# Optimization experiments

Measured on AMD Instinct MI355X. Metric: run time of the kernel, lower is better.

Reference implementation:

```python
import jax, jax.numpy as jnp
import numpy as np

D_MODEL, D_STATE, D_CONV, D_INNER = 1024, 16, 4, 2048
BATCH, SEQ = 4, 2048


def silu(v):
    return v * jax.nn.sigmoid(v)


def setup_inputs() -> dict:
    key = jax.random.key(0)
    ks = jax.random.split(key, 7)
    x = jax.random.normal(ks[0], (BATCH, SEQ, D_MODEL), dtype=jnp.float32)
    s = 0.02
    W_in = jax.random.normal(ks[1], (D_MODEL, 2 * D_INNER), dtype=jnp.float32) * s
    conv_w = jax.random.normal(ks[2], (D_INNER, 1, D_CONV), dtype=jnp.float32) * s  # depthwise (O, I/g=1, K)
    conv_b = jax.random.normal(ks[3], (D_INNER,), dtype=jnp.float32) * s
    W_xproj = jax.random.normal(ks[4], (D_INNER, 2 * D_STATE + 1), dtype=jnp.float32) * s
    A_log = jnp.log(jnp.tile(jnp.arange(1, D_STATE + 1, dtype=jnp.float32), (D_INNER, 1)))
    D = jnp.ones((D_INNER,), dtype=jnp.float32)
    W_out = jax.random.normal(ks[5], (D_INNER, D_MODEL), dtype=jnp.float32) * s
    return {"x": x, "W_in": W_in, "conv_w": conv_w, "conv_b": conv_b,
            "W_xproj": W_xproj, "A_log": A_log, "D": D, "W_out": W_out}


def reference(x, W_in, conv_w, conv_b, W_xproj, A_log, D, W_out):
    B, L, _ = x.shape
    xz = x @ W_in                                   # (B, L, 2*d_inner)
    x_proj, z = jnp.split(xz, 2, axis=-1)
    # Depthwise causal conv: padding=d_conv-1 then truncate to L == left-pad only.
    xc = jax.lax.conv_general_dilated(
        x_proj.transpose(0, 2, 1), conv_w,
        window_strides=(1,), padding=[(D_CONV - 1, 0)],
        feature_group_count=D_INNER,
        dimension_numbers=("NCH", "OIH", "NCH"))
    x_conv = silu((xc + conv_b[None, :, None]).transpose(0, 2, 1))  # (B, L, d_inner)
    ssm = x_conv @ W_xproj                           # (B, L, 1+2*d_state)
    delta = jax.nn.softplus(ssm[..., 0])             # (B, L)
    Bm = ssm[..., 1:1 + D_STATE]                     # (B, L, d_state)
    Cm = ssm[..., 1 + D_STATE:]                      # (B, L, d_state)
    # Original: deltaA = exp(delta*A) and softmax weights are computed but unused.
    deltaB = delta[..., None] * Bm                   # (B, L, d_state)
    # h_approx = mean_L(x outer deltaB): avoid (B,L,d_inner,d_state) intermediate.
    h_mean = jnp.einsum("bld,bln->bdn", x_conv, deltaB) / L  # (B, d_inner, d_state)
    y = jnp.einsum("bdn,bln->bld", h_mean, Cm)       # (B, L, d_inner)
    y = y + D[None, None, :] * x_conv
    y = y * silu(z)
    return y @ W_out                                 # (B, L, d_model)
```

## Files before the change

kernel.cpp:

```cpp
#include <hip/hip_runtime.h>
#include <hip/hip_bf16.h>
#include <stdint.h>

typedef __bf16 bf16x8 __attribute__((ext_vector_type(8)));
typedef float f32x4 __attribute__((ext_vector_type(4)));
typedef unsigned short u16;
typedef u16 ushort4v __attribute__((ext_vector_type(4)));
typedef u16 ushort8v __attribute__((ext_vector_type(8)));

__device__ __forceinline__ u16 f2bf(float f) {
    union { float f; uint32_t u; } v; v.f = f;
    uint32_t u = v.u + 0x7FFFu + ((v.u >> 16) & 1u);
    return (u16)(u >> 16);
}
__device__ __forceinline__ float bf2f(u16 b) {
    union { uint32_t u; float f; } v; v.u = ((uint32_t)b) << 16;
    return v.f;
}
__device__ __forceinline__ float silu_f(float v) {
    return v / (1.0f + __expf(-v));
}
__device__ __forceinline__ void gload_lds16(const u16* g, u16* l) {
    __builtin_amdgcn_global_load_lds(
        (const __attribute__((address_space(1))) void*)g,
        (__attribute__((address_space(3))) void*)l, 16, 0, 0);
}

__global__ void cvt_bf16_k(const float* __restrict__ src, u16* __restrict__ dst, int n4) {
    int i = blockIdx.x * 256 + threadIdx.x;
    if (i < n4) {
        float4 v = *(const float4*)&src[(int64_t)i * 4];
        ushort4v o = { f2bf(v.x), f2bf(v.y), f2bf(v.z), f2bf(v.w) };
        *(ushort4v*)&dst[(int64_t)i * 4] = o;
    }
}

__global__ __launch_bounds__(256) void trans_cvt_k(
        const float* __restrict__ src, u16* __restrict__ dst, int R, int C) {
    __shared__ float t[32][33];
    const int bc = blockIdx.x, br = blockIdx.y;
    const int tx = threadIdx.x & 31, ty = threadIdx.x >> 5;
#pragma unroll
    for (int i = 0; i < 4; i++) {
        int r = ty + i * 8;
        t[r][tx] = src[(int64_t)(br * 32 + r) * C + bc * 32 + tx];
    }
    __syncthreads();
#pragma unroll
    for (int i = 0; i < 4; i++) {
        int c = ty + i * 8;
        dst[(int64_t)(bc * 32 + c) * R + br * 32 + tx] = f2bf(t[tx][c]);
    }
}

__global__ void prep_wxt_k(const float* __restrict__ wx, u16* __restrict__ wxt) {
    int idx = blockIdx.x * 256 + threadIdx.x;
    if (idx < 48 * 2048) {
        int j = idx >> 11, d = idx & 2047;
        wxt[idx] = (j < 33) ? f2bf(wx[d * 33 + j]) : (u16)0;
    }
}

template<int M_REP, int WARPS_M, int B_HALVES, bool OUT_BF16>
__global__ __launch_bounds__(512) void gemm_dp(
        const u16* __restrict__ A, const u16* __restrict__ Bt,
        void* __restrict__ Cout, int nbn_sh, int NT, int lda, int ldb, int ldc) {
    constexpr int WARPS_N = 8 / WARPS_M;
    constexpr int QPT = M_REP / 2;
    constexpr int WV_M = M_REP * 16;
    constexpr int BN = WARPS_N * 64;
    constexpr int B_T = BN * 64;

    __shared__ __align__(16) u16 As[2 * 16384];
    __shared__ __align__(16) u16 Bs[2 * B_T];

    const int tid = threadIdx.x;
    const int wave = tid >> 6;
    const int lane = tid & 63;
    const int wm = wave / WARPS_N, wn = wave % WARPS_N;
    const int fr = lane & 15, fq = lane >> 4;

    const int nwg = gridDim.x;
    const int cpx = nwg >> 3;
    const int swz = (blockIdx.x & 7) * cpx + (blockIdx.x >> 3);
    const int bm = swz >> nbn_sh;
    const int bn = swz & ((1 << nbn_sh) - 1);

    const int srow = tid >> 3;
    const int scol8 = ((tid & 7) ^ (srow & 7)) * 8;
    const u16* gA = A + (int64_t)(bm * 256 + srow) * lda + scol8;
    const u16* gB = Bt + (int64_t)(bn * BN + srow) * ldb + scol8;
    const int64_t lda64 = lda, ldb64 = ldb;

    const int ksw0 = ((fq) ^ (fr & 7)) * 8;
    const int ksw1 = ((4 + fq) ^ (fr & 7)) * 8;
    const int arow0 = (wm * WV_M + fr) * 64;
    const int brow0 = (wn * 64 + fr) * 64;

    auto STAGE_A = [&](int kt, int buf) {
#pragma unroll
        for (int h = 0; h < 2; ++h)
#pragma unroll
            for (int j = 0; j < 2; ++j)
                gload_lds16(gA + (int64_t)(h * 128 + j * 64) * lda64 + kt * 64,
                            &As[buf * 16384 + h * 8192 + j * 4096 + tid * 8]);
    };
    auto STAGE_B_HALF = [&](int kt, int buf, int h) {
#pragma unroll
        for (int j = 0; j < 2; ++j)
            gload_lds16(gB + (int64_t)(h * 128 + j * 64) * ldb64 + kt * 64,
                        &Bs[buf * B_T + h * 8192 + j * 4096 + tid * 8]);
    };

    f32x4 acc[M_REP][4] = {};

    STAGE_A(0, 0);
#pragma unroll
    for (int h = 0; h < B_HALVES; ++h) STAGE_B_HALF(0, 0, h);
#pragma unroll
    for (int h = 0; h < B_HALVES; ++h) STAGE_B_HALF(1, 1, h);
    if constexpr (B_HALVES == 2) { asm volatile("s_waitcnt vmcnt(4)" ::: "memory"); }
    else                         { asm volatile("s_waitcnt vmcnt(2)" ::: "memory"); }
    __builtin_amdgcn_s_barrier();

    const int NI = NT >> 1;
    for (int s = 0; s < NI; ++s) {
        const bool more = (s + 1 < NI);
        const int kt2 = 2 * s + 2, kt3 = 2 * s + 3;
#pragma unroll
        for (int t = 0; t < 2; ++t) {
            const u16* Ab = &As[t * 16384];
            const u16* Bb = &Bs[t * B_T];
            bf16x8 breg[4][2];
#pragma unroll
            for (int q = 0; q < QPT; ++q) {
                if (q == 0) {
#pragma unroll
                    for (int n = 0; n < 4; ++n) {
                        breg[n][0] = *(const bf16x8*)(Bb + brow0 + n * 1024 + ksw0);
                        breg[n][1] = *(const bf16x8*)(Bb + brow0 + n * 1024 + ksw1);
                    }
                }
                bf16x8 areg[2][2];
#pragma unroll
                for (int j = 0; j < 2; ++j) {
                    areg[j][0] = *(const bf16x8*)(Ab + arow0 + (2 * q + j) * 1024 + ksw0);
                    areg[j][1] = *(const bf16x8*)(Ab + arow0 + (2 * q + j) * 1024 + ksw1);
                }
                if constexpr (QPT == 4) {
                    if (t == 0 && q == 0)         STAGE_A(2 * s + 1, 1);
                    if (t == 0 && q == 2 && more) STAGE_B_HALF(kt2, 0, 0);
                    if (t == 0 && q == 3 && more) STAGE_B_HALF(kt2, 0, 1);
                    if (t == 1 && q == 0 && more) STAGE_A(kt2, 0);
                    if (t == 1 && q == 2 && more) STAGE_B_HALF(kt3, 1, 0);
                    if (t == 1 && q == 3 && more) STAGE_B_HALF(kt3, 1, 1);
                } else {
                    if (t == 0 && q == 0)         STAGE_A(2 * s + 1, 1);
                    if (t == 0 && q == 1 && more) STAGE_B_HALF(kt2, 0, 0);
                    if (t == 1 && q == 0 && more) STAGE_A(kt2, 0);
                    if (t == 1 && q == 1 && more) STAGE_B_HALF(kt3, 1, 0);
                }
                __builtin_amdgcn_s_barrier();
                asm volatile("s_waitcnt lgkmcnt(0)" ::: "memory");
                __builtin_amdgcn_sched_barrier(0);
                __builtin_amdgcn_s_setprio(1);
#pragma unroll
                for (int j = 0; j < 2; ++j)
#pragma unroll
                    for (int n = 0; n < 4; ++n) {
                        acc[2 * q + j][n] = __builtin_amdgcn_mfma_f32_16x16x32_bf16(
                            areg[j][0], breg[n][0], acc[2 * q + j][n], 0, 0, 0);
                        acc[2 * q + j][n] = __builtin_amdgcn_mfma_f32_16x16x32_bf16(
                            areg[j][1], breg[n][1], acc[2 * q + j][n], 0, 0, 0);
                    }
                __builtin_amdgcn_s_setprio(0);
                __builtin_amdgcn_sched_barrier(0);
                if (q == QPT - 1) {
                    if (more) {
                        if constexpr (B_HALVES == 2) { asm volatile("s_waitcnt vmcnt(4)" ::: "memory"); }
                        else                         { asm volatile("s_waitcnt vmcnt(2)" ::: "memory"); }
                    } else {
                        asm volatile("s_waitcnt vmcnt(0)" ::: "memory");
                    }
                }
                __builtin_amdgcn_s_barrier();
            }
        }
    }

#pragma unroll
    for (int m = 0; m < M_REP; ++m) {
#pragma unroll
        for (int n = 0; n < 4; ++n) {
            const int col = bn * BN + wn * 64 + n * 16 + fr;
#pragma unroll
            for (int r = 0; r < 4; ++r) {
                const int row = bm * 256 + wm * WV_M + m * 16 + fq * 4 + r;
                if constexpr (OUT_BF16)
                    ((u16*)Cout)[(int64_t)row * ldc + col] = f2bf(acc[m][n][r]);
                else
                    ((float*)Cout)[(int64_t)row * ldc + col] = acc[m][n][r];
            }
        }
    }
}

__global__ __launch_bounds__(256) void conv_silu_k(
        const u16* __restrict__ xz, const float* __restrict__ cw,
        const float* __restrict__ cb, u16* __restrict__ xc) {
    const int blk = blockIdx.x;
    const int b = blk >> 9;
    const int l0 = (blk & 511) << 2;
    const int d0 = threadIdx.x * 8;
    float w[8][4], bias[8];
#pragma unroll
    for (int j = 0; j < 8; j++) {
        float4 wv = *(const float4*)&cw[(d0 + j) * 4];
        w[j][0] = wv.x; w[j][1] = wv.y; w[j][2] = wv.z; w[j][3] = wv.w;
        bias[j] = cb[d0 + j];
    }
    float xp[7][8];
#pragma unroll
    for (int r = 0; r < 7; r++) {
        int l = l0 - 3 + r;
        if (l < 0) {
#pragma unroll
            for (int j = 0; j < 8; j++) xp[r][j] = 0.f;
        } else {
            ushort8v v = *(const ushort8v*)&xz[((int64_t)(b * 2048 + l)) * 4096 + d0];
#pragma unroll
            for (int j = 0; j < 8; j++) xp[r][j] = bf2f(v[j]);
        }
    }
#pragma unroll
    for (int li = 0; li < 4; li++) {
        ushort8v o;
#pragma unroll
        for (int j = 0; j < 8; j++) {
            float s = bias[j];
#pragma unroll
            for (int k = 0; k < 4; k++) s += w[j][k] * xp[li + k][j];
            o[j] = f2bf(silu_f(s));
        }
        *(ushort8v*)&xc[((int64_t)(b * 2048 + l0 + li)) * 2048 + d0] = o;
    }
}

__global__ __launch_bounds__(256) void ssm_proj_k(
        const u16* __restrict__ xc, const u16* __restrict__ wxt,
        float* __restrict__ spart) {
    const int gw = (blockIdx.x << 2) + (threadIdx.x >> 6);
    const int lane = threadIdx.x & 63;
    const int rb = gw >> 2, kc = gw & 3;
    const int fr = lane & 15, fq = lane >> 4;
    const u16* ap = xc + (int64_t)(rb * 16 + fr) * 2048 + kc * 512 + fq * 8;
    const u16* bp = wxt + (int64_t)fr * 2048 + kc * 512 + fq * 8;
    f32x4 acc0 = {}, acc1 = {}, acc2 = {};
#pragma unroll 4
    for (int k = 0; k < 512; k += 32) {
        bf16x8 av = *(const bf16x8*)(ap + k);
        bf16x8 b0 = *(const bf16x8*)(bp + k);
        bf16x8 b1 = *(const bf16x8*)(bp + 16 * 2048 + k);
        bf16x8 b2 = *(const bf16x8*)(bp + 32 * 2048 + k);
        acc0 = __builtin_amdgcn_mfma_f32_16x16x32_bf16(av, b0, acc0, 0, 0, 0);
        acc1 = __builtin_amdgcn_mfma_f32_16x16x32_bf16(av, b1, acc1, 0, 0, 0);
        acc2 = __builtin_amdgcn_mfma_f32_16x16x32_bf16(av, b2, acc2, 0, 0, 0);
    }
    float* sp = spart + ((int64_t)kc * 8192 + rb * 16) * 48;
#pragma unroll
    for (int r = 0; r < 4; r++) {
        int ro = (fq * 4 + r) * 48;
        sp[ro + fr] = acc0[r];
        sp[ro + 16 + fr] = acc1[r];
        sp[ro + 32 + fr] = acc2[r];
    }
}

__global__ __launch_bounds__(256) void ssm_fin_k(
        const float* __restrict__ spart, float* __restrict__ dB,
        float* __restrict__ Cm) {
    const int row = blockIdx.x * 256 + threadIdx.x;
    const float* sp = spart + (int64_t)row * 48;
    float s[33];
#pragma unroll
    for (int j = 0; j < 33; j++)
        s[j] = sp[j] + sp[8192 * 48 + j] + sp[2 * 8192 * 48 + j] + sp[3 * 8192 * 48 + j];
    float d0v = s[0];
    float delta = (d0v > 20.f) ? d0v : log1pf(__expf(d0v));
#pragma unroll
    for (int n = 0; n < 16; n++) {
        dB[(int64_t)row * 16 + n] = delta * s[1 + n] * (1.0f / 2048.0f);
        Cm[(int64_t)row * 16 + n] = s[17 + n];
    }
}

__global__ __launch_bounds__(256) void h_part_k(
        const u16* __restrict__ xc, const float* __restrict__ dB,
        float* __restrict__ hp) {
    const int blk = blockIdx.x;
    const int dt = blk & 7, b = (blk >> 3) & 3, lc = blk >> 5;
    const int d = dt * 256 + threadIdx.x;
    const u16* xp = xc + ((int64_t)(b * 2048 + lc * 256)) * 2048 + d;
    const float* dbp = dB + (int64_t)(b * 2048 + lc * 256) * 16;
    float acc[16] = {};
    for (int l = 0; l < 256; l++) {
        float xv = bf2f(xp[(int64_t)l * 2048]);
#pragma unroll
        for (int n = 0; n < 16; n++) acc[n] += xv * dbp[l * 16 + n];
    }
    float* o = hp + ((int64_t)((lc * 4 + b) * 2048 + d)) * 16;
#pragma unroll
    for (int n = 0; n < 16; n++) o[n] = acc[n];
}

__global__ void h_red_k(const float* __restrict__ hp, float* __restrict__ h) {
    const int i = blockIdx.x * 256 + threadIdx.x;
    float s = 0.f;
#pragma unroll
    for (int c = 0; c < 8; c++) s += hp[(int64_t)c * 131072 + i];
    h[i] = s;
}

__global__ __launch_bounds__(256) void y_gate_k(
        u16* __restrict__ xz, const u16* __restrict__ xc,
        const float* __restrict__ h, const float* __restrict__ Cm,
        const float* __restrict__ Dp) {
    const int blk = blockIdx.x;
    const int lc = blk & 63, dt = (blk >> 6) & 1, b = blk >> 7;
    const int d0 = dt * 1024 + threadIdx.x * 4;
    const float* hpp = h + ((int64_t)(b * 2048 + d0)) * 16;
    float hreg[4][16];
#pragma unroll
    for (int i = 0; i < 4; i++)
#pragma unroll
        for (int n = 0; n < 16; n++) hreg[i][n] = hpp[i * 16 + n];
    float Dv[4];
#pragma unroll
    for (int i = 0; i < 4; i++) Dv[i] = Dp[d0 + i];
    __shared__ float Cs[32][16];
    if (threadIdx.x < 128)
        ((float4*)&Cs[0][0])[threadIdx.x] =
            ((const float4*)(Cm + (int64_t)(b * 2048 + lc * 32) * 16))[threadIdx.x];
    __syncthreads();
    for (int li = 0; li < 32; li++) {
        const int64_t rowz = (int64_t)(b * 2048 + lc * 32 + li);
        ushort4v xcv = *(const ushort4v*)&xc[rowz * 2048 + d0];
        ushort4v zv = *(const ushort4v*)&xz[rowz * 4096 + 2048 + d0];
        ushort4v o;
#pragma unroll
        for (int i = 0; i < 4; i++) {
            float s = Dv[i] * bf2f(xcv[i]);
#pragma unroll
            for (int n = 0; n < 16; n++) s += hreg[i][n] * Cs[li][n];
            o[i] = f2bf(s * silu_f(bf2f(zv[i])));
        }
        *(ushort4v*)&xz[rowz * 4096 + d0] = o;
    }
}

extern "C" void kernel_launch(void* const* d_in, const int* in_sizes, int n_in,
                              void* d_out, int out_size, void* d_ws, size_t ws_size,
                              hipStream_t stream) {
    (void)in_sizes; (void)n_in; (void)out_size; (void)ws_size;
    const float* x      = (const float*)d_in[0];
    const float* W_in   = (const float*)d_in[1];
    const float* conv_w = (const float*)d_in[2];
    const float* conv_b = (const float*)d_in[3];
    const float* W_xp   = (const float*)d_in[4];
    const float* Dp     = (const float*)d_in[6];
    const float* W_out  = (const float*)d_in[7];
    float* out = (float*)d_out;
    char* ws = (char*)d_ws;

    u16*   x_bf   = (u16*)(ws);
    float* spart  = (float*)(ws);
    float* dB     = (float*)(ws + 6291456);
    float* Cm     = (float*)(ws + 6815744);
    float* hp     = (float*)(ws + 7340032);
    float* h      = (float*)(ws + 11534336);
    u16*   Wt_in  = (u16*)(ws + 16777216);
    u16*   Wt_out = (u16*)(ws + 25165824);
    u16*   Wxt    = (u16*)(ws + 29360128);
    u16*   xz     = (u16*)(ws + 29556736);
    u16*   xcv    = (u16*)(ws + 96665600);

    cvt_bf16_k<<<8192, 256, 0, stream>>>(x, x_bf, 2097152);
    trans_cvt_k<<<dim3(128, 32), 256, 0, stream>>>(W_in, Wt_in, 1024, 4096);
    trans_cvt_k<<<dim3(32, 64), 256, 0, stream>>>(W_out, Wt_out, 2048, 1024);
    prep_wxt_k<<<384, 256, 0, stream>>>(W_xp, Wxt);
    gemm_dp<8, 2, 2, true><<<512, 512, 0, stream>>>(x_bf, Wt_in, xz, 4, 16, 1024, 1024, 4096);
    conv_silu_k<<<2048, 256, 0, stream>>>(xz, conv_w, conv_b, xcv);
    ssm_proj_k<<<512, 256, 0, stream>>>(xcv, Wxt, spart);
    ssm_fin_k<<<32, 256, 0, stream>>>(spart, dB, Cm);
    h_part_k<<<256, 256, 0, stream>>>(xcv, dB, hp);
    h_red_k<<<512, 256, 0, stream>>>(hp, h);
    y_gate_k<<<512, 256, 0, stream>>>(xz, xcv, h, Cm, Dp);
    gemm_dp<4, 4, 1, false><<<256, 512, 0, stream>>>(xz, Wt_out, out, 3, 32, 4096, 2048, 1024);
}
```

Measured before the change: 250.7 us.

## Fuse prep kernels into one launch and split A staging into halves

Merges the four weight/input conversion kernels into a single prep_k launch that dispatches on block index, removing three kernel launches. In the GEMM, A-tile staging is split into two halves spread across q iterations so global-to-LDS traffic is more evenly interleaved with MFMA work. LDS fragment reads now use inline ds_read_b128 asm on 32-bit addresses. The inline asm is volatile and may constrain compiler scheduling, and the split staging changes the outstanding load counts that the waits depend on.

```diff
diff --git a/kernel.cpp b/kernel.cpp
--- a/kernel.cpp
+++ b/kernel.cpp
@@ -25,37 +25,45 @@
         (const __attribute__((address_space(1))) void*)g,
         (__attribute__((address_space(3))) void*)l, 16, 0, 0);
 }
-
-__global__ void cvt_bf16_k(const float* __restrict__ src, u16* __restrict__ dst, int n4) {
-    int i = blockIdx.x * 256 + threadIdx.x;
-    if (i < n4) {
-        float4 v = *(const float4*)&src[(int64_t)i * 4];
+__device__ __forceinline__ bf16x8 lds_read16(uint32_t addr) {
+    bf16x8 r;
+    asm volatile("ds_read_b128 %0, %1" : "=v"(r) : "v"(addr));
+    return r;
+}
+
+__device__ __forceinline__ void trans_tile(
+        const float* __restrict__ src, u16* __restrict__ dst, int R, int C,
+        int bc, int br, float (*tt)[33], int tid) {
+    const int tx = tid & 31, ty = tid >> 5;
+#pragma unroll
+    for (int i = 0; i < 4; i++)
+        tt[ty + i * 8][tx] = src[(int64_t)(br * 32 + ty + i * 8) * C + bc * 32 + tx];
+    __syncthreads();
+#pragma unroll
+    for (int i = 0; i < 4; i++)
+        dst[(int64_t)(bc * 32 + ty + i * 8) * R + br * 32 + tx] = f2bf(tt[tx][ty + i * 8]);
+}
+
+__global__ __launch_bounds__(256) void prep_k(
+        const float* __restrict__ x, u16* __restrict__ x_bf,
+        const float* __restrict__ Wi, u16* __restrict__ Wti,
+        const float* __restrict__ Wo, u16* __restrict__ Wto,
+        const float* __restrict__ wx, u16* __restrict__ wxt) {
+    __shared__ float tt[32][33];
+    const int blk = blockIdx.x, tid = threadIdx.x;
+    if (blk < 8192) {
+        int i = blk * 256 + tid;
+        float4 v = *(const float4*)&x[(int64_t)i * 4];
         ushort4v o = { f2bf(v.x), f2bf(v.y), f2bf(v.z), f2bf(v.w) };
-        *(ushort4v*)&dst[(int64_t)i * 4] = o;
-    }
-}
-
-__global__ __launch_bounds__(256) void trans_cvt_k(
-        const float* __restrict__ src, u16* __restrict__ dst, int R, int C) {
-    __shared__ float t[32][33];
-    const int bc = blockIdx.x, br = blockIdx.y;
-    const int tx = threadIdx.x & 31, ty = threadIdx.x >> 5;
-#pragma unroll
-    for (int i = 0; i < 4; i++) {
-        int r = ty + i * 8;
-        t[r][tx] = src[(int64_t)(br * 32 + r) * C + bc * 32 + tx];
-    }
-    __syncthreads();
-#pragma unroll
-    for (int i = 0; i < 4; i++) {
-        int c = ty + i * 8;
-        dst[(int64_t)(bc * 32 + c) * R + br * 32 + tx] = f2bf(t[tx][c]);
-    }
-}
-
-__global__ void prep_wxt_k(const float* __restrict__ wx, u16* __restrict__ wxt) {
-    int idx = blockIdx.x * 256 + threadIdx.x;
-    if (idx < 48 * 2048) {
+        *(ushort4v*)&x_bf[(int64_t)i * 4] = o;
+    } else if (blk < 12288) {
+        int t = blk - 8192;
+        trans_tile(Wi, Wti, 1024, 4096, t & 127, t >> 7, tt, tid);
+    } else if (blk < 14336) {
+        int t = blk - 12288;
+        trans_tile(Wo, Wto, 2048, 1024, t & 31, t >> 5, tt, tid);
+    } else {
+        int idx = (blk - 14336) * 256 + tid;
         int j = idx >> 11, d = idx & 2047;
         wxt[idx] = (j < 33) ? f2bf(wx[d * 33 + j]) : (u16)0;
     }
@@ -73,6 +81,8 @@
 
     __shared__ __align__(16) u16 As[2 * 16384];
     __shared__ __align__(16) u16 Bs[2 * B_T];
+    const uint32_t asb = (uint32_t)(uintptr_t)&As[0];
+    const uint32_t bsb = (uint32_t)(uintptr_t)&Bs[0];
 
     const int tid = threadIdx.x;
     const int wave = tid >> 6;
@@ -97,13 +107,11 @@
     const int arow0 = (wm * WV_M + fr) * 64;
     const int brow0 = (wn * 64 + fr) * 64;
 
-    auto STAGE_A = [&](int kt, int buf) {
-#pragma unroll
-        for (int h = 0; h < 2; ++h)
-#pragma unroll
-            for (int j = 0; j < 2; ++j)
-                gload_lds16(gA + (int64_t)(h * 128 + j * 64) * lda64 + kt * 64,
-                            &As[buf * 16384 + h * 8192 + j * 4096 + tid * 8]);
+    auto STAGE_A_HALF = [&](int kt, int buf, int h) {
+#pragma unroll
+        for (int j = 0; j < 2; ++j)
+            gload_lds16(gA + (int64_t)(h * 128 + j * 64) * lda64 + kt * 64,
+                        &As[buf * 16384 + h * 8192 + j * 4096 + tid * 8]);
     };
     auto STAGE_B_HALF = [&](int kt, int buf, int h) {
 #pragma unroll
@@ -114,7 +122,7 @@
 
     f32x4 acc[M_REP][4] = {};
 
-    STAGE_A(0, 0);
+    STAGE_A_HALF(0, 0, 0); STAGE_A_HALF(0, 0, 1);
 #pragma unroll
     for (int h = 0; h < B_HALVES; ++h) STAGE_B_HALF(0, 0, h);
 #pragma unroll
@@ -126,39 +134,42 @@
     const int NI = NT >> 1;
     for (int s = 0; s < NI; ++s) {
         const bool more = (s + 1 < NI);
-        const int kt2 = 2 * s + 2, kt3 = 2 * s + 3;
 #pragma unroll
         for (int t = 0; t < 2; ++t) {
-            const u16* Ab = &As[t * 16384];
-            const u16* Bb = &Bs[t * B_T];
+            const uint32_t Ab = asb + t * 32768u;
+            const uint32_t Bb = bsb + t * (uint32_t)(B_T * 2);
             bf16x8 breg[4][2];
 #pragma unroll
             for (int q = 0; q < QPT; ++q) {
                 if (q == 0) {
 #pragma unroll
                     for (int n = 0; n < 4; ++n) {
-                        breg[n][0] = *(const bf16x8*)(Bb + brow0 + n * 1024 + ksw0);
-                        breg[n][1] = *(const bf16x8*)(Bb + brow0 + n * 1024 + ksw1);
+                        breg[n][0] = lds_read16(Bb + (uint32_t)(brow0 + n * 1024 + ksw0) * 2);
+                        breg[n][1] = lds_read16(Bb + (uint32_t)(brow0 + n * 1024 + ksw1) * 2);
                     }
                 }
                 bf16x8 areg[2][2];
 #pragma unroll
                 for (int j = 0; j < 2; ++j) {
-                    areg[j][0] = *(const bf16x8*)(Ab + arow0 + (2 * q + j) * 1024 + ksw0);
-                    areg[j][1] = *(const bf16x8*)(Ab + arow0 + (2 * q + j) * 1024 + ksw1);
+                    areg[j][0] = lds_read16(Ab + (uint32_t)(arow0 + (2 * q + j) * 1024 + ksw0) * 2);
+                    areg[j][1] = lds_read16(Ab + (uint32_t)(arow0 + (2 * q + j) * 1024 + ksw1) * 2);
                 }
                 if constexpr (QPT == 4) {
-                    if (t == 0 && q == 0)         STAGE_A(2 * s + 1, 1);
-                    if (t == 0 && q == 2 && more) STAGE_B_HALF(kt2, 0, 0);
-                    if (t == 0 && q == 3 && more) STAGE_B_HALF(kt2, 0, 1);
-                    if (t == 1 && q == 0 && more) STAGE_A(kt2, 0);
-                    if (t == 1 && q == 2 && more) STAGE_B_HALF(kt3, 1, 0);
-                    if (t == 1 && q == 3 && more) STAGE_B_HALF(kt3, 1, 1);
+                    if (t == 0 && q == 0)         STAGE_A_HALF(2 * s + 1, 1, 0);
+                    if (t == 0 && q == 1)         STAGE_A_HALF(2 * s + 1, 1, 1);
+                    if (t == 0 && q == 2 && more) STAGE_B_HALF(2 * s + 2, 0, 0);
+                    if (t == 0 && q == 3 && more) STAGE_B_HALF(2 * s + 2, 0, 1);
+                    if (t == 1 && q == 0 && more) STAGE_A_HALF(2 * s + 2, 0, 0);
+                    if (t == 1 && q == 1 && more) STAGE_A_HALF(2 * s + 2, 0, 1);
+                    if (t == 1 && q == 2 && more) STAGE_B_HALF(2 * s + 3, 1, 0);
+                    if (t == 1 && q == 3 && more) STAGE_B_HALF(2 * s + 3, 1, 1);
                 } else {
-                    if (t == 0 && q == 0)         STAGE_A(2 * s + 1, 1);
-                    if (t == 0 && q == 1 && more) STAGE_B_HALF(kt2, 0, 0);
-                    if (t == 1 && q == 0 && more) STAGE_A(kt2, 0);
-                    if (t == 1 && q == 1 && more) STAGE_B_HALF(kt3, 1, 0);
+                    if (t == 0 && q == 0)         STAGE_A_HALF(2 * s + 1, 1, 0);
+                    if (t == 0 && q == 1) {       STAGE_A_HALF(2 * s + 1, 1, 1);
+                        if (more)                 STAGE_B_HALF(2 * s + 2, 0, 0); }
+                    if (t == 1 && q == 0 && more) STAGE_A_HALF(2 * s + 2, 0, 0);
+                    if (t == 1 && q == 1 && more) { STAGE_A_HALF(2 * s + 2, 0, 1);
+                                                    STAGE_B_HALF(2 * s + 3, 1, 0); }
                 }
                 __builtin_amdgcn_s_barrier();
                 asm volatile("s_waitcnt lgkmcnt(0)" ::: "memory");
@@ -384,10 +395,7 @@
     u16*   xz     = (u16*)(ws + 29556736);
     u16*   xcv    = (u16*)(ws + 96665600);
 
-    cvt_bf16_k<<<8192, 256, 0, stream>>>(x, x_bf, 2097152);
-    trans_cvt_k<<<dim3(128, 32), 256, 0, stream>>>(W_in, Wt_in, 1024, 4096);
-    trans_cvt_k<<<dim3(32, 64), 256, 0, stream>>>(W_out, Wt_out, 2048, 1024);
-    prep_wxt_k<<<384, 256, 0, stream>>>(W_xp, Wxt);
+    prep_k<<<14720, 256, 0, stream>>>(x, x_bf, W_in, Wt_in, W_out, Wt_out, W_xp, Wxt);
     gemm_dp<8, 2, 2, true><<<512, 512, 0, stream>>>(x_bf, Wt_in, xz, 4, 16, 1024, 1024, 4096);
     conv_silu_k<<<2048, 256, 0, stream>>>(xz, conv_w, conv_b, xcv);
     ssm_proj_k<<<512, 256, 0, stream>>>(xcv, Wxt, spart);
```

After: 244.1 us. 1.03x faster.
